# Optimization experiments

Hardware: AMD Instinct MI355X
Metric: run time of the kernel (lower is better)

Reference implementation:

```python
import jax, jax.numpy as jnp
import numpy as np
from jax import lax

B, C, H, W = 4, 512, 64, 64
C8 = C // 8
OUT = 256
BN_EPS = 1e-5


def setup_inputs() -> dict:
    key = jax.random.key(0)
    ks = jax.random.split(key, 12)
    s = lambda k, shape, fan: jax.random.normal(k, shape, jnp.float32) * (1.0 / np.sqrt(fan))
    return {
        "x": jax.random.normal(ks[0], (B, C, H, W), jnp.float32),
        "wq": s(ks[1], (C8, C), C), "bq": jnp.zeros((C8,), jnp.float32),
        "wk": s(ks[2], (C8, C), C), "bk": jnp.zeros((C8,), jnp.float32),
        "wv": s(ks[3], (C, C), C),  "bv": jnp.zeros((C,), jnp.float32),
        "ca_w1": s(ks[4], (C8, C), C),
        "ca_w2": s(ks[5], (C, C8), C8),
        "conv_w": s(ks[6], (OUT, C, 3, 3), C * 9),
        "bn_gamma": jnp.ones((OUT,), jnp.float32),
        "bn_beta": jnp.zeros((OUT,), jnp.float32),
        "bn_mean": jnp.zeros((OUT,), jnp.float32),
        "bn_var": jnp.ones((OUT,), jnp.float32),
    }


def reference(x, wq, bq, wk, bk, wv, bv, ca_w1, ca_w2, conv_w,
              bn_gamma, bn_beta, bn_mean, bn_var):
    b, c, h, w = x.shape
    n = h * w
    xf = x.reshape(b, c, n)  # [B,C,N]

    # ---- Position attention ----
    q = jnp.einsum('qc,bcn->bnq', wq, xf) + bq            # [B,N,C8]
    k = jnp.einsum('kc,bcn->bkn', wk, xf) + bk[:, None]   # [B,C8,N]
    energy = jnp.einsum('bnq,bqm->bnm', q, k)             # [B,N,N]
    attn = jax.nn.softmax(energy, axis=-1)
    v = jnp.einsum('vc,bcn->bvn', wv, xf) + bv[:, None]   # [B,C,N]
    # torch: bmm(value, attention^T) -> out[b,c,m] = sum_n v[b,c,n]*attn[b,m,n]
    pa = jnp.einsum('bcn,bmn->bcm', v, attn).reshape(b, c, h, w) + x

    # ---- Channel attention (SE-style, avg+max pooled, shared MLP) ----
    avg = jnp.mean(pa, axis=(2, 3))   # [B,C]
    mx = jnp.max(pa, axis=(2, 3))     # [B,C]
    fc = lambda z: jnp.einsum('oc,bc->bo', ca_w2,
                              jax.nn.relu(jnp.einsum('hc,bc->bh', ca_w1, z)))
    scale = jax.nn.sigmoid(fc(avg) + fc(mx))[:, :, None, None]
    ca = scale * pa

    # ---- Conv 3x3 + BN (eval mode) + ReLU ----
    y = lax.conv_general_dilated(ca, conv_w, (1, 1), 'SAME',
                                 dimension_numbers=('NCHW', 'OIHW', 'NCHW'))
    inv = lax.rsqrt(bn_var + BN_EPS)
    y = (y - bn_mean[:, None, None]) * (inv * bn_gamma)[:, None, None] + bn_beta[:, None, None]
    return jax.nn.relu(y)
```

## Files before the change

kernel.cpp:

```cpp
#include <hip/hip_runtime.h>

#define NB 4
#define CIN 512
#define NPIX 4096
#define CQK 64
#define COUT 256
#define PPIX 4356

typedef __bf16 bh16;
typedef _Float16 fh16;
typedef __attribute__((ext_vector_type(8))) __bf16 bf16x8;
typedef __attribute__((ext_vector_type(8))) _Float16 f16x8;
typedef __attribute__((ext_vector_type(16))) float f32x16;

#define AS1 __attribute__((address_space(1)))
#define AS3 __attribute__((address_space(3)))

__device__ __forceinline__ void glds16(const void* g, void* l) {
  __builtin_amdgcn_global_load_lds((const AS1 unsigned int*)g, (AS3 unsigned int*)l, 16, 0, 0);
}

__global__ __launch_bounds__(256) void transpose_bf_k(const float* __restrict__ src,
                                                      bh16* __restrict__ dst,
                                                      int rows, int cols) {
  __shared__ float tile[32][33];
  const int b = blockIdx.z;
  const int c0 = blockIdx.x * 32;
  const int r0 = blockIdx.y * 32;
  const float* s = src + (size_t)b * rows * cols;
  bh16* d = dst + (size_t)b * rows * cols;
  const int tx = threadIdx.x, ty = threadIdx.y;
#pragma unroll
  for (int i = 0; i < 32; i += 8)
    tile[ty + i][tx] = s[(size_t)(r0 + ty + i) * cols + (c0 + tx)];
  __syncthreads();
#pragma unroll
  for (int i = 0; i < 32; i += 8)
    d[(size_t)(c0 + ty + i) * rows + (r0 + tx)] = (bh16)tile[tx][ty + i];
}

__global__ __launch_bounds__(256) void wcast_k(const float* __restrict__ wq,
                                               const float* __restrict__ wk,
                                               const float* __restrict__ wv,
                                               const float* __restrict__ bq,
                                               const float* __restrict__ bk,
                                               bh16* __restrict__ Wqk,
                                               bh16* __restrict__ wvb,
                                               float* __restrict__ bias128) {
  const int idx = blockIdx.x * 256 + threadIdx.x;
  if (idx < 65536) {
    Wqk[idx] = (bh16)(idx < 32768 ? wq[idx] : wk[idx - 32768]);
  } else {
    const int j = idx - 65536;
    wvb[j] = (bh16)wv[j];
  }
  if (idx < 128) bias128[idx] = idx < 64 ? bq[idx] : bk[idx - 64];
}

__global__ __launch_bounds__(256) void qk_proj_k(const bh16* __restrict__ xTb,
                                                 const bh16* __restrict__ Wqk,
                                                 const float* __restrict__ bias128,
                                                 bh16* __restrict__ Qb,
                                                 bh16* __restrict__ Kf) {
  const int blk = blockIdx.x;
  const int t = threadIdx.x;
  const int w = t >> 6, l31 = t & 31, hi = (t & 63) >> 5;
  __shared__ __align__(16) bh16 As[2][64 * 64];
  f32x16 acc[2];
#pragma unroll
  for (int nt = 0; nt < 2; nt++)
#pragma unroll
    for (int r = 0; r < 16; r++) acc[nt][r] = 0.0f;

#define QK_STAGE(kc, buf)                                                           \
  {                                                                                 \
    _Pragma("unroll") for (int i = 0; i < 2; i++) {                                 \
      const int s = i * 256 + t;                                                    \
      const int n = s >> 3, slot = s & 7;                                           \
      glds16(xTb + (size_t)(blk * 64 + n) * CIN + (kc) * 64 + (((slot + n) & 7) * 8), \
             &As[buf][(size_t)(i * 256 + w * 64) * 8]);                             \
    }                                                                               \
  }

  QK_STAGE(0, 0);
  __syncthreads();
  for (int kc = 0; kc < 8; kc++) {
    if (kc < 7) QK_STAGE(kc + 1, (kc + 1) & 1);
    const bh16* as = As[kc & 1];
#pragma unroll
    for (int ks = 0; ks < 4; ks++) {
      const bf16x8 bfr = *(const bf16x8*)(Wqk + (size_t)(w * 32 + l31) * CIN + kc * 64 + ks * 16 + hi * 8);
      const int kk = ks * 2 + hi;
#pragma unroll
      for (int nt = 0; nt < 2; nt++) {
        const int n = nt * 32 + l31;
        const bf16x8 a = *(const bf16x8*)&as[(size_t)(n * 8 + ((kk - n) & 7)) * 8];
        acc[nt] = __builtin_amdgcn_mfma_f32_32x32x16_bf16(a, bfr, acc[nt], 0, 0, 0);
      }
    }
    __syncthreads();
  }
#undef QK_STAGE
  const int o = w * 32 + l31;
  const float bo = bias128[o];
  if (w < 2) {
#pragma unroll
    for (int nt = 0; nt < 2; nt++)
#pragma unroll
      for (int r = 0; r < 16; r++) {
        const int nloc = nt * 32 + (r & 3) + 8 * (r >> 2) + 4 * hi;
        Qb[(size_t)(blk * 64 + nloc) * 64 + o] = (bh16)(acc[nt][r] + bo);
      }
  } else {
    const int b = blk >> 6, jtile = blk & 63;
    const int k = o - 64, kg = k >> 3, k7 = k & 7;
    bh16* kdst = Kf + (((size_t)(b * 64 + jtile) * 8 + kg) * 64) * 8 + k7;
#pragma unroll
    for (int nt = 0; nt < 2; nt++)
#pragma unroll
      for (int r = 0; r < 16; r++) {
        const int j = nt * 32 + (r & 3) + 8 * (r >> 2) + 4 * hi;
        kdst[(size_t)j * 8] = (bh16)(acc[nt][r] + bo);
      }
  }
}

__global__ __launch_bounds__(256) void v_proj_k(const bh16* __restrict__ xTb,
                                                const bh16* __restrict__ wvb,
                                                const float* __restrict__ bv,
                                                bh16* __restrict__ Vf) {
  const int nblk = blockIdx.x;
  const int cblk = blockIdx.y;
  const int b = blockIdx.z;
  const int t = threadIdx.x;
  const int w = t >> 6, l31 = t & 31, hi = (t & 63) >> 5;
  __shared__ __align__(16) bh16 Bs[2][256 * 64];
  f32x16 acc[2][2];
#pragma unroll
  for (int mt = 0; mt < 2; mt++)
#pragma unroll
    for (int nt = 0; nt < 2; nt++)
#pragma unroll
      for (int r = 0; r < 16; r++) acc[mt][nt][r] = 0.0f;

#define V_STAGE(kc, buf)                                                              \
  {                                                                                   \
    _Pragma("unroll") for (int i = 0; i < 8; i++) {                                   \
      const int s = i * 256 + t;                                                      \
      const int n = s >> 3, slot = s & 7;                                             \
      glds16(xTb + (size_t)(b * NPIX + nblk * 256 + n) * CIN + (kc) * 64 + (((slot + n) & 7) * 8), \
             &Bs[buf][(size_t)(i * 256 + w * 64) * 8]);                               \
    }                                                                                 \
  }

  V_STAGE(0, 0);
  __syncthreads();
  for (int kc = 0; kc < 8; kc++) {
    if (kc < 7) V_STAGE(kc + 1, (kc + 1) & 1);
    const bh16* bs = Bs[kc & 1];
#pragma unroll
    for (int ks = 0; ks < 4; ks++) {
      const int kk = ks * 2 + hi;
      bf16x8 a[2], bfr[2];
#pragma unroll
      for (int mt = 0; mt < 2; mt++)
        a[mt] = *(const bf16x8*)(wvb + (size_t)(cblk * 64 + mt * 32 + l31) * CIN + kc * 64 + ks * 16 + hi * 8);
#pragma unroll
      for (int nt = 0; nt < 2; nt++) {
        const int n = w * 64 + nt * 32 + l31;
        bfr[nt] = *(const bf16x8*)&bs[(size_t)(n * 8 + ((kk - n) & 7)) * 8];
      }
#pragma unroll
      for (int mt = 0; mt < 2; mt++)
#pragma unroll
        for (int nt = 0; nt < 2; nt++)
          acc[mt][nt] = __builtin_amdgcn_mfma_f32_32x32x16_bf16(a[mt], bfr[nt], acc[mt][nt], 0, 0, 0);
    }
    __syncthreads();
  }
#undef V_STAGE
  const int ntile0 = nblk * 4 + w;
#pragma unroll
  for (int mt = 0; mt < 2; mt++)
#pragma unroll
    for (int r = 0; r < 16; r++) {
      const int c = cblk * 64 + mt * 32 + (r & 3) + 8 * (r >> 2) + 4 * hi;
      const float bvc = bv[c];
#pragma unroll
      for (int nt = 0; nt < 2; nt++) {
        const int nl = nt * 32 + l31;
        Vf[(((size_t)(b * 64 + ntile0) * 8 + (nl >> 3)) * 512 + c) * 8 + (nl & 7)] =
            (bh16)(acc[mt][nt][r] + bvc);
      }
    }
}

__global__ __launch_bounds__(256, 2) void attn1p_k(const bh16* __restrict__ Qb,
                                                   const bh16* __restrict__ Kf,
                                                   const bh16* __restrict__ Vf,
                                                   const float* __restrict__ x,
                                                   float* __restrict__ pa) {
  const int id = blockIdx.x + 2 * (blockIdx.y + 64 * blockIdx.z);
  const int b = (id & 7) >> 1;
  const int cblk = id & 1;
  const int mblk = (id >> 3) * 64;
  const int t = threadIdx.x;
  const int w = t >> 6, l31 = t & 31, hi = (t >> 5) & 1;
  const int jhalf = w & 1, mhalf = w >> 1;
  __shared__ __align__(16) bh16 Ps[2][8 * 64 * 8];
  __shared__ float lred[4][32];
  __shared__ float linvL[64];

  bf16x8 qf[4];
  {
    const bh16* qrow = Qb + (size_t)(b * NPIX + mblk + mhalf * 32 + l31) * 64;
#pragma unroll
    for (int ks = 0; ks < 4; ks++) qf[ks] = *(const bf16x8*)(qrow + ks * 16 + hi * 8);
  }
  const bh16* kfb = Kf + (size_t)b * (64 * 8 * 64 * 8);
  const bh16* vfb = Vf + (size_t)b * (64 * 8 * 512 * 8);
  const int cbase = cblk * 256 + w * 64;

#define KADDR(tile, ks) (kfb + (((size_t)(tile) * 8 + (ks) * 2 + hi) * 64 + jhalf * 32 + l31) * 8)
#define VADDR(tile, ks, ct) (vfb + (((size_t)(tile) * 8 + (ks) * 2 + hi) * 512 + cbase + (ct) * 32 + l31) * 8)

  f32x16 acc[2][2];
#pragma unroll
  for (int mt = 0; mt < 2; mt++)
#pragma unroll
    for (int ct = 0; ct < 2; ct++)
#pragma unroll
      for (int r = 0; r < 16; r++) acc[mt][ct][r] = 0.0f;
  float lsum = 0.0f;

  bf16x8 kf_nxt[4], kf_fly[4];
  bf16x8 vf_use[4][2], vf_rdy[4][2];
  f32x16 s1;
  {
    bf16x8 k0[4];
#pragma unroll
    for (int ks = 0; ks < 4; ks++) {
      k0[ks] = *(const bf16x8*)KADDR(0, ks);
#pragma unroll
      for (int ct = 0; ct < 2; ct++) vf_rdy[ks][ct] = *(const bf16x8*)VADDR(0, ks, ct);
    }
#pragma unroll
    for (int ks = 0; ks < 4; ks++) {
      kf_nxt[ks] = *(const bf16x8*)KADDR(1, ks);
      kf_fly[ks] = *(const bf16x8*)KADDR(2, ks);
    }
#pragma unroll
    for (int r = 0; r < 16; r++) s1[r] = 0.0f;
#pragma unroll
    for (int ks = 0; ks < 4; ks++)
      s1 = __builtin_amdgcn_mfma_f32_32x32x16_bf16(k0[ks], qf[ks], s1, 0, 0, 0);
  }

  for (int it = 0; it < 64; it++) {
    f32x16 s1n;
#pragma unroll
    for (int r = 0; r < 16; r++) s1n[r] = 0.0f;
#pragma unroll
    for (int ks = 0; ks < 4; ks++)
      s1n = __builtin_amdgcn_mfma_f32_32x32x16_bf16(kf_nxt[ks], qf[ks], s1n, 0, 0, 0);

    const bh16* ps = Ps[(it + 1) & 1];
    bh16* psw = Ps[it & 1];
    if (it) {
#pragma unroll
      for (int ks = 0; ks < 4; ks++) {
        bf16x8 pf0 = *(const bf16x8*)&ps[(size_t)((ks * 2 + hi) * 64 + l31) * 8];
        bf16x8 pf1 = *(const bf16x8*)&ps[(size_t)((ks * 2 + hi) * 64 + 32 + l31) * 8];
        acc[0][0] = __builtin_amdgcn_mfma_f32_32x32x16_bf16(pf0, vf_use[ks][0], acc[0][0], 0, 0, 0);
        acc[0][1] = __builtin_amdgcn_mfma_f32_32x32x16_bf16(pf0, vf_use[ks][1], acc[0][1], 0, 0, 0);
        {
          union { bh16 h[4]; uint2 u2; } pk;
#pragma unroll
          for (int q = 0; q < 4; q++) {
            const float p = __expf(s1[ks * 4 + q]);
            lsum += p;
            pk.h[q] = (bh16)p;
          }
          *(uint2*)(void*)&psw[(size_t)((jhalf * 4 + ks) * 64 + mhalf * 32 + l31) * 8 + hi * 4] = pk.u2;
        }
        acc[1][0] = __builtin_amdgcn_mfma_f32_32x32x16_bf16(pf1, vf_use[ks][0], acc[1][0], 0, 0, 0);
        acc[1][1] = __builtin_amdgcn_mfma_f32_32x32x16_bf16(pf1, vf_use[ks][1], acc[1][1], 0, 0, 0);
      }
    } else {
#pragma unroll
      for (int g = 0; g < 4; g++) {
        union { bh16 h[4]; uint2 u2; } pk;
#pragma unroll
        for (int q = 0; q < 4; q++) {
          const float p = __expf(s1[g * 4 + q]);
          lsum += p;
          pk.h[q] = (bh16)p;
        }
        *(uint2*)(void*)&psw[(size_t)((jhalf * 4 + g) * 64 + mhalf * 32 + l31) * 8 + hi * 4] = pk.u2;
      }
    }
    __syncthreads();
    s1 = s1n;
    const int kt = (it + 3 < 64) ? it + 3 : 63;
    const int vt = (it + 1 < 64) ? it + 1 : 63;
#pragma unroll
    for (int ks = 0; ks < 4; ks++) {
      kf_nxt[ks] = kf_fly[ks];
      kf_fly[ks] = *(const bf16x8*)KADDR(kt, ks);
      vf_use[ks][0] = vf_rdy[ks][0];
      vf_use[ks][1] = vf_rdy[ks][1];
      vf_rdy[ks][0] = *(const bf16x8*)VADDR(vt, ks, 0);
      vf_rdy[ks][1] = *(const bf16x8*)VADDR(vt, ks, 1);
    }
  }
  {
    const bh16* ps = Ps[1];
#pragma unroll
    for (int ks = 0; ks < 4; ks++) {
      bf16x8 pf0 = *(const bf16x8*)&ps[(size_t)((ks * 2 + hi) * 64 + l31) * 8];
      bf16x8 pf1 = *(const bf16x8*)&ps[(size_t)((ks * 2 + hi) * 64 + 32 + l31) * 8];
      acc[0][0] = __builtin_amdgcn_mfma_f32_32x32x16_bf16(pf0, vf_use[ks][0], acc[0][0], 0, 0, 0);
      acc[0][1] = __builtin_amdgcn_mfma_f32_32x32x16_bf16(pf0, vf_use[ks][1], acc[0][1], 0, 0, 0);
      acc[1][0] = __builtin_amdgcn_mfma_f32_32x32x16_bf16(pf1, vf_use[ks][0], acc[1][0], 0, 0, 0);
      acc[1][1] = __builtin_amdgcn_mfma_f32_32x32x16_bf16(pf1, vf_use[ks][1], acc[1][1], 0, 0, 0);
    }
  }
#undef KADDR
#undef VADDR

  lsum += __shfl_xor(lsum, 32);
  if (hi == 0) lred[w][l31] = lsum;
  __syncthreads();
  if (t < 64) linvL[t] = 1.0f / (lred[(t >> 5) * 2][t & 31] + lred[(t >> 5) * 2 + 1][t & 31]);
  __syncthreads();

#pragma unroll
  for (int mt = 0; mt < 2; mt++) {
#pragma unroll
    for (int g = 0; g < 4; g++) {
      const int mloc = mt * 32 + g * 8 + hi * 4;
      const float4 lv = *(const float4*)&linvL[mloc];
#pragma unroll
      for (int ct = 0; ct < 2; ct++) {
        const size_t base = (size_t)(b * CIN + cblk * 256 + w * 64 + ct * 32 + l31) * NPIX + mblk + mloc;
        const float4 xv = *(const float4*)&x[base];
        float4 r;
        r.x = acc[mt][ct][g * 4 + 0] * lv.x + xv.x;
        r.y = acc[mt][ct][g * 4 + 1] * lv.y + xv.y;
        r.z = acc[mt][ct][g * 4 + 2] * lv.z + xv.z;
        r.w = acc[mt][ct][g * 4 + 3] * lv.w + xv.w;
        *(float4*)&pa[base] = r;
      }
    }
  }
}

__global__ __launch_bounds__(256) void pool2_k(const float* __restrict__ pa,
                                               float* __restrict__ avgv,
                                               float* __restrict__ maxv) {
  const int t = threadIdx.x;
  const int row = blockIdx.x * 4 + (t >> 6);
  const int lane = t & 63;
  const float* base = pa + (size_t)row * NPIX;
  float s = 0.0f, mx = -1e30f;
#pragma unroll
  for (int i = 0; i < 16; i++) {
    const float4 v = *(const float4*)(base + i * 256 + lane * 4);
    s += v.x + v.y + v.z + v.w;
    mx = fmaxf(mx, fmaxf(fmaxf(v.x, v.y), fmaxf(v.z, v.w)));
  }
#pragma unroll
  for (int d = 1; d < 64; d <<= 1) {
    s += __shfl_xor(s, d);
    mx = fmaxf(mx, __shfl_xor(mx, d));
  }
  if (lane == 0) {
    avgv[row] = s * (1.0f / 4096.0f);
    maxv[row] = mx;
  }
}

__global__ __launch_bounds__(256) void mlp2_k(const float* __restrict__ avgv,
                                              const float* __restrict__ maxv,
                                              const float* __restrict__ w1,
                                              const float* __restrict__ w2,
                                              float* __restrict__ scale) {
  const int b = blockIdx.x;
  const int t = threadIdx.x;
  __shared__ float avg_l[CIN], max_l[CIN], hbuf[128];
#pragma unroll
  for (int h = 0; h < 2; h++) {
    const int c = t + h * 256;
    avg_l[c] = avgv[b * CIN + c];
    max_l[c] = maxv[b * CIN + c];
  }
  __syncthreads();
  if (t < 128) {
    const float* src = (t < 64) ? avg_l : max_l;
    const int o = t & 63;
    float sacc = 0.0f;
    for (int c = 0; c < CIN; c++) sacc += w1[o * CIN + c] * src[c];
    hbuf[t] = fmaxf(sacc, 0.0f);
  }
  __syncthreads();
#pragma unroll
  for (int h = 0; h < 2; h++) {
    const int c = t + h * 256;
    float sacc = 0.0f;
#pragma unroll
    for (int k = 0; k < 64; k++) sacc += w2[c * 64 + k] * (hbuf[k] + hbuf[64 + k]);
    scale[b * CIN + c] = 1.0f / (1.0f + __expf(-sacc));
  }
}

__global__ __launch_bounds__(256) void pack_k(const float* __restrict__ pa,
                                              const float* __restrict__ scl,
                                              fh16* __restrict__ pab) {
  __shared__ float tile[32][65];
  const int n0 = blockIdx.x * 32;
  const int c0 = blockIdx.y * 64;
  const int b = blockIdx.z;
  const int t = threadIdx.x;
  {
    const int px = t & 31, cc = t >> 5;
#pragma unroll
    for (int i = 0; i < 8; i++) {
      const int c = cc * 8 + i;
      tile[px][c] = pa[((size_t)(b * CIN + c0 + c)) * NPIX + n0 + px] * scl[b * CIN + c0 + c];
    }
  }
  __syncthreads();
  {
    const int pixr = t >> 5, c2 = (t & 31) * 2;
#pragma unroll
    for (int j = 0; j < 4; j++) {
      const int pix = pixr + j * 8;
      const int n = n0 + pix;
      const int pp = ((n >> 6) + 1) * 66 + (n & 63) + 1;
      union { fh16 h[2]; unsigned int u; } pk;
      pk.h[0] = (fh16)tile[pix][c2];
      pk.h[1] = (fh16)tile[pix][c2 + 1];
      *(unsigned int*)(void*)(pab + ((size_t)b * PPIX + pp) * CIN + c0 + c2) = pk.u;
    }
  }
}

__global__ __launch_bounds__(256) void wpack_k(const float* __restrict__ cw,
                                               fh16* __restrict__ wp) {
  const int d0 = (blockIdx.x * 256 + threadIdx.x) * 8;
  const int cc = d0 & 15;
  const int q = d0 >> 4;
  const int o = q & 63;
  const int q2 = q >> 6;
  const int tap = q2 % 9;
  const int q3 = q2 / 9;
  const int chunk = q3 & 31;
  const int oblk = q3 >> 5;
  const size_t sbase = (size_t)(oblk * 64 + o) * 4608 + (size_t)(chunk * 16 + cc) * 9 + tap;
  union { fh16 h[8]; uint4 u4; } pk;
#pragma unroll
  for (int i = 0; i < 8; i++) pk.h[i] = (fh16)cw[sbase + (size_t)i * 9];
  *(uint4*)(void*)(wp + d0) = pk.u4;
}

__global__ __launch_bounds__(256) void conv_mfma_k(const fh16* __restrict__ pab,
                                                   const fh16* __restrict__ wp,
                                                   const float* __restrict__ gamma,
                                                   const float* __restrict__ beta,
                                                   const float* __restrict__ mean,
                                                   const float* __restrict__ var,
                                                   float* __restrict__ out) {
  const int y0 = blockIdx.x * 4;
  const int oblk = blockIdx.y;
  const int b = blockIdx.z;
  const int t = threadIdx.x;
  const int w = t >> 6, lane = t & 63, l31 = lane & 31, hi = lane >> 5;
  __shared__ __align__(16) fh16 Xs[2][416 * 16];
  __shared__ __align__(16) fh16 Ws[2][9 * 64 * 16];
  __shared__ float sb[64], bb[64];
  if (t < 64) {
    const int o = oblk * 64 + t;
    const float inv = rsqrtf(var[o] + 1e-5f);
    const float sc = inv * gamma[o];
    sb[t] = sc;
    bb[t] = beta[o] - mean[o] * sc;
  }
  f32x16 o00, o01, o10, o11;
#pragma unroll
  for (int r = 0; r < 16; r++) { o00[r] = 0.0f; o01[r] = 0.0f; o10[r] = 0.0f; o11[r] = 0.0f; }

  const fh16* xbase = pab + ((size_t)b * PPIX + y0 * 66) * CIN + (lane >> 1) * CIN + (lane & 1) * 8;
  const fh16* wbase = wp + (size_t)oblk * 32 * 9216 + lane * 8;

#define STAGE(chunk, buf)                                                        \
  {                                                                              \
    const fh16* xs = xbase + (chunk) * 16;                                       \
    for (int i = w; i < 13; i += 4)                                              \
      glds16(xs + (size_t)i * 32 * CIN, &Xs[buf][i * 512]);                      \
    const fh16* wsrc = wbase + (size_t)(chunk) * 9216;                           \
    for (int i = w; i < 18; i += 4)                                              \
      glds16(wsrc + (size_t)i * 512, &Ws[buf][i * 512]);                         \
  }

  STAGE(0, 0);
  __syncthreads();
  for (int chunk = 0; chunk < 32; chunk++) {
    if (chunk < 31) STAGE(chunk + 1, (chunk + 1) & 1);
    const fh16* xs = Xs[chunk & 1];
    const fh16* ws = Ws[chunk & 1];
#pragma unroll
    for (int tap = 0; tap < 9; tap++) {
      const int ky = tap / 3, kx = tap - ky * 3;
      const f16x8 a0 = *(const f16x8*)&ws[tap * 1024 + l31 * 16 + hi * 8];
      const f16x8 a1 = *(const f16x8*)&ws[tap * 1024 + (32 + l31) * 16 + hi * 8];
      const int px = ((w + ky) * 66 + l31 + kx) * 16 + hi * 8;
      const f16x8 b0 = *(const f16x8*)&xs[px];
      const f16x8 b1 = *(const f16x8*)&xs[px + 32 * 16];
      o00 = __builtin_amdgcn_mfma_f32_32x32x16_f16(a0, b0, o00, 0, 0, 0);
      o01 = __builtin_amdgcn_mfma_f32_32x32x16_f16(a0, b1, o01, 0, 0, 0);
      o10 = __builtin_amdgcn_mfma_f32_32x32x16_f16(a1, b0, o10, 0, 0, 0);
      o11 = __builtin_amdgcn_mfma_f32_32x32x16_f16(a1, b1, o11, 0, 0, 0);
    }
    __syncthreads();
  }
#undef STAGE

  const f32x16* accs[2][2] = {{&o00, &o01}, {&o10, &o11}};
#pragma unroll
  for (int mt = 0; mt < 2; mt++) {
#pragma unroll
    for (int nt = 0; nt < 2; nt++) {
      const f32x16& A = *accs[mt][nt];
#pragma unroll
      for (int r = 0; r < 16; r++) {
        const int cl = mt * 32 + (r & 3) + 8 * (r >> 2) + 4 * hi;
        const int pix = nt * 32 + l31;
        const float y = A[r] * sb[cl] + bb[cl];
        out[((size_t)(b * COUT + oblk * 64 + cl)) * NPIX + (y0 + w) * 64 + pix] = fmaxf(y, 0.0f);
      }
    }
  }
}

extern "C" void kernel_launch(void* const* d_in, const int* in_sizes, int n_in,
                              void* d_out, int out_size, void* d_ws, size_t ws_size,
                              hipStream_t stream) {
  (void)in_sizes; (void)n_in; (void)out_size; (void)ws_size;
  const float* x        = (const float*)d_in[0];
  const float* wq       = (const float*)d_in[1];
  const float* bq       = (const float*)d_in[2];
  const float* wk       = (const float*)d_in[3];
  const float* bk       = (const float*)d_in[4];
  const float* wv       = (const float*)d_in[5];
  const float* bv       = (const float*)d_in[6];
  const float* ca_w1    = (const float*)d_in[7];
  const float* ca_w2    = (const float*)d_in[8];
  const float* conv_w   = (const float*)d_in[9];
  const float* bn_gamma = (const float*)d_in[10];
  const float* bn_beta  = (const float*)d_in[11];
  const float* bn_mean  = (const float*)d_in[12];
  const float* bn_var   = (const float*)d_in[13];
  float* out = (float*)d_out;

  float* ws = (float*)d_ws;
  float* pa      = ws;
  bh16*  Vf      = (bh16*)(ws + 8388608);
  fh16*  wpck    = (fh16*)(ws + 8388608);
  bh16*  Qb      = (bh16*)(ws + 12582912);
  bh16*  Kf      = (bh16*)(ws + 13107200);
  bh16*  xTb     = (bh16*)(ws + 13631488);
  fh16*  pab     = (fh16*)(ws + 13631488);
  bh16*  Wqk     = (bh16*)(ws + 17825792);
  bh16*  wvb     = (bh16*)(ws + 17858560);
  float* bias128 = ws + 17989632;
  float* avgv    = ws + 18100224;
  float* maxv    = ws + 18102272;
  float* scl     = ws + 18104320;

  wcast_k<<<dim3(1280, 1, 1), 256, 0, stream>>>(wq, wk, wv, bq, bk, Wqk, wvb, bias128);
  transpose_bf_k<<<dim3(NPIX / 32, CIN / 32, NB), dim3(32, 8, 1), 0, stream>>>(x, xTb, CIN, NPIX);
  qk_proj_k<<<dim3(256, 1, 1), 256, 0, stream>>>(xTb, Wqk, bias128, Qb, Kf);
  v_proj_k<<<dim3(16, 8, NB), 256, 0, stream>>>(xTb, wvb, bv, Vf);
  attn1p_k<<<dim3(2, 64, NB), 256, 0, stream>>>(Qb, Kf, Vf, x, pa);
  hipMemsetAsync(pab, 0, (size_t)(NB * PPIX * CIN + 16384) * sizeof(fh16), stream);
  pool2_k<<<dim3(512, 1, 1), 256, 0, stream>>>(pa, avgv, maxv);
  mlp2_k<<<dim3(NB, 1, 1), 256, 0, stream>>>(avgv, maxv, ca_w1, ca_w2, scl);
  pack_k<<<dim3(NPIX / 32, CIN / 64, NB), 256, 0, stream>>>(pa, scl, pab);
  wpack_k<<<dim3(576, 1, 1), 256, 0, stream>>>(conv_w, wpck);
  conv_mfma_k<<<dim3(16, 4, NB), 256, 0, stream>>>(pab, wpck, bn_gamma, bn_beta,
                                                   bn_mean, bn_var, out);
}
```

Baseline: 344.6 us.

## Use exp2 softmax, split sum accumulators, zero only halo, and relayout conv LDS tiles

```diff
diff --git a/kernel.cpp b/kernel.cpp
--- a/kernel.cpp
+++ b/kernel.cpp
@@ -18,6 +18,14 @@
 
 __device__ __forceinline__ void glds16(const void* g, void* l) {
   __builtin_amdgcn_global_load_lds((const AS1 unsigned int*)g, (AS3 unsigned int*)l, 16, 0, 0);
+}
+
+__device__ __forceinline__ float fexp2(float x) {
+#if __has_builtin(__builtin_amdgcn_exp2f)
+  return __builtin_amdgcn_exp2f(x);
+#else
+  return __expf(x * 0.6931471805599453f);
+#endif
 }
 
 __global__ __launch_bounds__(256) void transpose_bf_k(const float* __restrict__ src,
@@ -109,7 +117,7 @@
 #pragma unroll
       for (int r = 0; r < 16; r++) {
         const int nloc = nt * 32 + (r & 3) + 8 * (r >> 2) + 4 * hi;
-        Qb[(size_t)(blk * 64 + nloc) * 64 + o] = (bh16)(acc[nt][r] + bo);
+        Qb[(size_t)(blk * 64 + nloc) * 64 + o] = (bh16)((acc[nt][r] + bo) * 1.44269504088896f);
       }
   } else {
     const int b = blk >> 6, jtile = blk & 63;
@@ -231,7 +239,8 @@
     for (int ct = 0; ct < 2; ct++)
 #pragma unroll
       for (int r = 0; r < 16; r++) acc[mt][ct][r] = 0.0f;
-  float lsum = 0.0f;
+  float4 lsacc;
+  lsacc.x = 0.0f; lsacc.y = 0.0f; lsacc.z = 0.0f; lsacc.w = 0.0f;
 
   bf16x8 kf_nxt[4], kf_fly[4];
   bf16x8 vf_use[4][2], vf_rdy[4][2];
@@ -256,7 +265,9 @@
       s1 = __builtin_amdgcn_mfma_f32_32x32x16_bf16(k0[ks], qf[ks], s1, 0, 0, 0);
   }
 
+#pragma unroll 2
   for (int it = 0; it < 64; it++) {
+    __builtin_amdgcn_s_setprio(1);
     f32x16 s1n;
 #pragma unroll
     for (int r = 0; r < 16; r++) s1n[r] = 0.0f;
@@ -277,8 +288,8 @@
           union { bh16 h[4]; uint2 u2; } pk;
 #pragma unroll
           for (int q = 0; q < 4; q++) {
-            const float p = __expf(s1[ks * 4 + q]);
-            lsum += p;
+            const float p = fexp2(s1[ks * 4 + q]);
+            lsacc[q] += p;
             pk.h[q] = (bh16)p;
           }
           *(uint2*)(void*)&psw[(size_t)((jhalf * 4 + ks) * 64 + mhalf * 32 + l31) * 8 + hi * 4] = pk.u2;
@@ -292,13 +303,14 @@
         union { bh16 h[4]; uint2 u2; } pk;
 #pragma unroll
         for (int q = 0; q < 4; q++) {
-          const float p = __expf(s1[g * 4 + q]);
-          lsum += p;
+          const float p = fexp2(s1[g * 4 + q]);
+          lsacc[q] += p;
           pk.h[q] = (bh16)p;
         }
         *(uint2*)(void*)&psw[(size_t)((jhalf * 4 + g) * 64 + mhalf * 32 + l31) * 8 + hi * 4] = pk.u2;
       }
     }
+    __builtin_amdgcn_s_setprio(0);
     __syncthreads();
     s1 = s1n;
     const int kt = (it + 3 < 64) ? it + 3 : 63;
@@ -328,6 +340,7 @@
 #undef KADDR
 #undef VADDR
 
+  float lsum = (lsacc.x + lsacc.y) + (lsacc.z + lsacc.w);
   lsum += __shfl_xor(lsum, 32);
   if (hi == 0) lred[w][l31] = lsum;
   __syncthreads();
@@ -445,22 +458,35 @@
   }
 }
 
+__global__ __launch_bounds__(256) void bzero_k(fh16* __restrict__ pab) {
+  const int t = threadIdx.x;
+  const int p = blockIdx.x * 4 + (t >> 6);
+  const int b = blockIdx.y;
+  int pp;
+  if (p < 66) pp = p;
+  else if (p < 132) pp = 65 * 66 + (p - 66);
+  else if (p < 196) pp = (p - 131) * 66;
+  else pp = (p - 195) * 66 + 65;
+  uint4 z = {0u, 0u, 0u, 0u};
+  *(uint4*)(void*)(pab + ((size_t)b * PPIX + pp) * CIN + (t & 63) * 8) = z;
+}
+
 __global__ __launch_bounds__(256) void wpack_k(const float* __restrict__ cw,
                                                fh16* __restrict__ wp) {
-  const int d0 = (blockIdx.x * 256 + threadIdx.x) * 8;
-  const int cc = d0 & 15;
-  const int q = d0 >> 4;
-  const int o = q & 63;
-  const int q2 = q >> 6;
-  const int tap = q2 % 9;
-  const int q3 = q2 / 9;
-  const int chunk = q3 & 31;
-  const int oblk = q3 >> 5;
-  const size_t sbase = (size_t)(oblk * 64 + o) * 4608 + (size_t)(chunk * 16 + cc) * 9 + tap;
-  union { fh16 h[8]; uint4 u4; } pk;
-#pragma unroll
-  for (int i = 0; i < 8; i++) pk.h[i] = (fh16)cw[sbase + (size_t)i * 9];
-  *(uint4*)(void*)(wp + d0) = pk.u4;
+  const int slot = blockIdx.x * 256 + threadIdx.x;
+  const int oblk = slot / 36864;
+  const int r1 = slot - oblk * 36864;
+  const int chunk = r1 / 1152;
+  const int r2 = r1 - chunk * 1152;
+  const int tap = r2 >> 7;
+  const int r3 = r2 & 127;
+  const int h = r3 >> 6;
+  const int o = r3 & 63;
+  const size_t sbase = (size_t)(oblk * 64 + o) * 4608 + (size_t)(chunk * 16 + h * 8) * 9 + tap;
+  union { fh16 h8[8]; uint4 u4; } pk;
+#pragma unroll
+  for (int i = 0; i < 8; i++) pk.h8[i] = (fh16)cw[sbase + (size_t)i * 9];
+  *(uint4*)(void*)(wp + (size_t)slot * 8) = pk.u4;
 }
 
 __global__ __launch_bounds__(256) void conv_mfma_k(const fh16* __restrict__ pab,
@@ -489,7 +515,7 @@
 #pragma unroll
   for (int r = 0; r < 16; r++) { o00[r] = 0.0f; o01[r] = 0.0f; o10[r] = 0.0f; o11[r] = 0.0f; }
 
-  const fh16* xbase = pab + ((size_t)b * PPIX + y0 * 66) * CIN + (lane >> 1) * CIN + (lane & 1) * 8;
+  const fh16* xbase = pab + ((size_t)b * PPIX + y0 * 66) * CIN + (size_t)(lane & 31) * CIN + (lane >> 5) * 8;
   const fh16* wbase = wp + (size_t)oblk * 32 * 9216 + lane * 8;
 
 #define STAGE(chunk, buf)                                                        \
@@ -511,11 +537,12 @@
 #pragma unroll
     for (int tap = 0; tap < 9; tap++) {
       const int ky = tap / 3, kx = tap - ky * 3;
-      const f16x8 a0 = *(const f16x8*)&ws[tap * 1024 + l31 * 16 + hi * 8];
-      const f16x8 a1 = *(const f16x8*)&ws[tap * 1024 + (32 + l31) * 16 + hi * 8];
-      const int px = ((w + ky) * 66 + l31 + kx) * 16 + hi * 8;
-      const f16x8 b0 = *(const f16x8*)&xs[px];
-      const f16x8 b1 = *(const f16x8*)&xs[px + 32 * 16];
+      const f16x8 a0 = *(const f16x8*)&ws[tap * 1024 + hi * 512 + l31 * 8];
+      const f16x8 a1 = *(const f16x8*)&ws[tap * 1024 + hi * 512 + (32 + l31) * 8];
+      const int row0 = (w + ky) * 66 + l31 + kx;
+      const int row1 = row0 + 32;
+      const f16x8 b0 = *(const f16x8*)&xs[(row0 >> 5) * 512 + hi * 256 + (row0 & 31) * 8];
+      const f16x8 b1 = *(const f16x8*)&xs[(row1 >> 5) * 512 + hi * 256 + (row1 & 31) * 8];
       o00 = __builtin_amdgcn_mfma_f32_32x32x16_f16(a0, b0, o00, 0, 0, 0);
       o01 = __builtin_amdgcn_mfma_f32_32x32x16_f16(a0, b1, o01, 0, 0, 0);
       o10 = __builtin_amdgcn_mfma_f32_32x32x16_f16(a1, b0, o10, 0, 0, 0);
@@ -582,7 +609,7 @@
   qk_proj_k<<<dim3(256, 1, 1), 256, 0, stream>>>(xTb, Wqk, bias128, Qb, Kf);
   v_proj_k<<<dim3(16, 8, NB), 256, 0, stream>>>(xTb, wvb, bv, Vf);
   attn1p_k<<<dim3(2, 64, NB), 256, 0, stream>>>(Qb, Kf, Vf, x, pa);
-  hipMemsetAsync(pab, 0, (size_t)(NB * PPIX * CIN + 16384) * sizeof(fh16), stream);
+  bzero_k<<<dim3(65, NB, 1), 256, 0, stream>>>(pab);
   pool2_k<<<dim3(512, 1, 1), 256, 0, stream>>>(pa, avgv, maxv);
   mlp2_k<<<dim3(NB, 1, 1), 256, 0, stream>>>(avgv, maxv, ca_w1, ca_w2, scl);
   pack_k<<<dim3(NPIX / 32, CIN / 64, NB), 256, 0, stream>>>(pa, scl, pab);
```

Result: slower. 449.7 us (+30.5%).
